# Kernel optimization log

Hardware: AMD Instinct MI355X
Metric: run time of the kernel (lower is better)

## Reference

```python
import jax, jax.numpy as jnp
import numpy as np

H, W = 64, 64
N = H * W                 # pixels
M_LOC = 2048              # unknown pixels for matting Laplacian
M_IU = 2048               # unknown pixels for intra-unknown term
NNZ_CM = 20 * N           # color-mixture nnz


def setup_inputs() -> dict:
    key = jax.random.key(0)
    k = jax.random.split(key, 15)
    inp = {}
    inp["height"] = H
    inp["width"] = W
    inp["CM_weights"] = jax.random.uniform(k[0], (N,), jnp.float32)
    inp["LOC_weights"] = jax.random.uniform(k[1], (N,), jnp.float32)
    inp["IU_weights"] = jax.random.uniform(k[2], (N,), jnp.float32)
    inp["KU_weights"] = jax.random.uniform(k[3], (N,), jnp.float32)
    inp["lmbda"] = jnp.float32(100.0)
    inp["kToUconf"] = jax.random.uniform(k[4], (N,), jnp.float32)
    inp["known"] = (jax.random.uniform(k[5], (N,)) < 0.5).astype(jnp.float32)
    inp["kToU"] = jax.random.uniform(k[6], (N,), jnp.float32)
    inp["Wcm_row"] = jax.random.randint(k[7], (NNZ_CM,), 0, N)
    inp["Wcm_col"] = jax.random.randint(k[8], (NNZ_CM,), 0, N)
    inp["Wcm_data"] = jax.random.uniform(k[9], (NNZ_CM,), jnp.float32)
    # interior pixels so all 3x3 neighbor offsets stay in [0, N)
    inp["LOC_inInd"] = jax.random.randint(k[10], (M_LOC, 1), W + 1, N - W - 1)
    inp["LOC_flows"] = jax.random.uniform(k[11], (9, 9, M_LOC), jnp.float32)
    inp["IU_inInd"] = jax.random.randint(k[12], (M_IU, 1), 0, N)
    inp["IU_flows"] = jax.random.uniform(k[13], (M_IU, 5), jnp.float32)
    inp["IU_neighInd"] = jax.random.randint(k[14], (M_IU, 5), 0, N)
    return inp


def _coo_dense(rows, cols, vals, n):
    # from_coo with duplicate (row, col) entries summed
    return jnp.zeros((n, n), vals.dtype).at[rows, cols].add(vals)


def reference(height, width, CM_weights, LOC_weights, IU_weights, KU_weights,
              lmbda, kToUconf, known, kToU, Wcm_row, Wcm_col, Wcm_data,
              LOC_inInd, LOC_flows, IU_inInd, IU_flows, IU_neighInd):
    n = height * width

    # ---- color mixture: Lcm = (diag(rowsum) - diag(cm) @ Wcm);  Lcm <- Lcm^T @ Lcm
    Wcm = _coo_dense(Wcm_row, Wcm_col, Wcm_data, n) * CM_weights[:, None]
    Lcm = jnp.diag(Wcm.sum(axis=1)) - Wcm
    Lcm = Lcm.T @ Lcm

    # ---- matting Laplacian (faithful to source: loop breaks after i == 0,
    # so only the first neighbor's rows/flows are scattered)
    w_loc = LOC_weights[LOC_inInd[:, 0]]                 # [M]
    flows = LOC_flows * w_loc[None, None, :]             # [9, 9, M]
    offs = jnp.array([-1 - width, -1, -1 + width, -width, 0, width,
                      1 - width, 1, 1 + width], dtype=LOC_inInd.dtype)
    neigh = LOC_inInd + offs[None, :]                    # [M, 9]
    m = neigh.shape[0]
    rows0 = jnp.broadcast_to(neigh[:, :1], (m, 9))       # neighInds[:, 0] tiled
    vals0 = flows[:, 0, :].T                             # [M, 9]
    Wmat = _coo_dense(rows0.reshape(-1), neigh.reshape(-1), vals0.reshape(-1), n)
    Wmat = 0.5 * (Wmat + Wmat.T)
    Lmat = jnp.diag(Wmat.sum(axis=1)) - Wmat

    # ---- intra-unknowns (5 nonlocal neighbors)
    w_iu = IU_weights[IU_inInd[:, 0]]                    # [Mi]
    f_iu = IU_flows[:, :5] * w_iu[:, None]               # [Mi, 5]
    mi = IU_inInd.shape[0]
    rows_iu = jnp.broadcast_to(IU_inInd, (mi, 5))
    Wcs = _coo_dense(rows_iu.reshape(-1), IU_neighInd[:, :5].reshape(-1),
                     f_iu.reshape(-1), n)
    Wcs = 0.5 * (Wcs + Wcs.T)
    Lcs = jnp.diag(Wcs.sum(axis=1)) - Wcs

    # ---- assemble linear system A x = b
    ku_diag = KU_weights * kToUconf
    known_diag = lmbda * known
    A = Lcs + Lmat + Lcm + jnp.diag(ku_diag + known_diag)
    b = (ku_diag + known_diag) * kToU
    return A, b
```

## Files before the change

kernel.cpp:

```cpp
#include <hip/hip_runtime.h>

#define WD 64
#define NN 4096
#define RCAP 128
#define XCAP 512

typedef float v4f __attribute__((ext_vector_type(4)));


__global__ void k_scatter(const int* __restrict__ wrow, const int* __restrict__ wcol,
                          const float* __restrict__ wdata, const float* __restrict__ cmw,
                          const int* __restrict__ locInd, const float* __restrict__ locFlows,
                          const float* __restrict__ locw,
                          const int* __restrict__ iuInd, const float* __restrict__ iuFlows,
                          const int* __restrict__ iuNeigh, const float* __restrict__ iuw,
                          int nnz, int mloc, int miu,
                          int* __restrict__ curR, int* __restrict__ curC, int* __restrict__ curX,
                          float* __restrict__ rowsum,
                          int2* __restrict__ sR, int2* __restrict__ sC, int2* __restrict__ xE) {
    int t = blockIdx.x * blockDim.x + threadIdx.x;
    if (t < nnz) {
        int r = wrow[t], c = wcol[t];
        float pos = wdata[t] * cmw[r];
        float v = -pos;
        atomicAdd(&rowsum[r], pos);
        int pR = atomicAdd(&curR[r], 1);
        if (pR < RCAP) sR[r * RCAP + pR] = make_int2(c, __float_as_int(v));
        int pC = atomicAdd(&curC[c], 1);
        if (pC < RCAP) sC[c * RCAP + pC] = make_int2(r, __float_as_int(v));
        return;
    }
    t -= nnz;
    if (t < mloc * 9) {
        int m = t / 9;
        int j = t - m * 9;
        const int offs[9] = {-1-WD, -1, -1+WD, -WD, 0, WD, 1-WD, 1, 1+WD};
        int ind = locInd[m];
        int r = ind - 1 - WD;
        int c = ind + offs[j];
        float h = 0.5f * locFlows[j * 9 * mloc + m] * locw[ind];
        int p1 = atomicAdd(&curX[r], 2);
        if (p1 + 1 < XCAP) {
            xE[r * XCAP + p1]     = make_int2(c, __float_as_int(-h));
            xE[r * XCAP + p1 + 1] = make_int2(r, __float_as_int( h));
        }
        int p2 = atomicAdd(&curX[c], 2);
        if (p2 + 1 < XCAP) {
            xE[c * XCAP + p2]     = make_int2(r, __float_as_int(-h));
            xE[c * XCAP + p2 + 1] = make_int2(c, __float_as_int( h));
        }
        return;
    }
    t -= mloc * 9;
    if (t < miu * 5) {
        int m = t / 5;
        int j = t - m * 5;
        int r = iuInd[m];
        int c = iuNeigh[m * 5 + j];
        float h = 0.5f * iuFlows[m * 5 + j] * iuw[r];
        int p1 = atomicAdd(&curX[r], 2);
        if (p1 + 1 < XCAP) {
            xE[r * XCAP + p1]     = make_int2(c, __float_as_int(-h));
            xE[r * XCAP + p1 + 1] = make_int2(r, __float_as_int( h));
        }
        int p2 = atomicAdd(&curX[c], 2);
        if (p2 + 1 < XCAP) {
            xE[c * XCAP + p2]     = make_int2(r, __float_as_int(-h));
            xE[c * XCAP + p2 + 1] = make_int2(c, __float_as_int( h));
        }
    }
}

__global__ void __launch_bounds__(256) k_rows(
    const int* __restrict__ curR, const int2* __restrict__ sR,
    const int* __restrict__ curC, const int2* __restrict__ sC,
    const int* __restrict__ curX, const int2* __restrict__ xE,
    const float* __restrict__ rowsum,
    const float* __restrict__ kuw, const float* __restrict__ conf, const float* __restrict__ known,
    const float* __restrict__ kToU, const float* __restrict__ lmbda,
    float* __restrict__ A, float* __restrict__ b) {
    __shared__ float acc[NN];
    __shared__ int   ck[RCAP + 1];
    __shared__ float cv[RCAP + 1];
    __shared__ int   crl[RCAP + 1];
    __shared__ float crs[RCAP + 1];
    int i = blockIdx.x;
    int tid = threadIdx.x;

    v4f* acc4 = (v4f*)acc;
    for (int t = tid; t < NN / 4; t += 256) acc4[t] = (v4f){0.f, 0.f, 0.f, 0.f};

    int ccnt = min(curC[i], RCAP);
    int ctot = ccnt + 1;
    for (int t = tid; t < ctot; t += 256) {
        int k; float v;
        if (t < ccnt) { int2 e = sC[i * RCAP + t]; k = e.x; v = __int_as_float(e.y); }
        else          { k = i;                     v = rowsum[i]; }
        ck[t] = k; cv[t] = v;
        crl[t] = min(curR[k], RCAP);
        crs[t] = rowsum[k];
    }
    __syncthreads();

    int wave = tid >> 6, lane = tid & 63;
    int sub = lane >> 5, hl = lane & 31;
    for (int kk = wave * 2 + sub; kk < ctot; kk += 8) {
        int k = ck[kk];
        float v = cv[kk];
        int rl = crl[kk];
        const int2* rowp = sR + k * RCAP;
        for (int t = hl; t <= rl; t += 32) {
            int j; float w;
            if (t < rl) { int2 e = rowp[t]; j = e.x; w = __int_as_float(e.y); }
            else        { j = k; w = crs[kk]; }
            atomicAdd(&acc[j], v * w);
        }
    }
    int xc = min(curX[i], XCAP);
    const int2* xp = xE + i * XCAP;
    for (int t = tid; t < xc; t += 256) {
        int2 e = xp[t];
        atomicAdd(&acc[e.x], __int_as_float(e.y));
    }
    if (tid == 0) {
        float d = kuw[i] * conf[i] + lmbda[0] * known[i];
        atomicAdd(&acc[i], d);
        b[i] = d * kToU[i];
    }
    __syncthreads();

    v4f* out4 = (v4f*)(A + (size_t)i * NN);
    for (int t = tid; t < NN / 4; t += 256)
        __builtin_nontemporal_store(acc4[t], &out4[t]);
}

extern "C" void kernel_launch(void* const* d_in, const int* in_sizes, int n_in,
                              void* d_out, int out_size, void* d_ws, size_t ws_size,
                              hipStream_t stream) {
    const float* CM_weights  = (const float*)d_in[2];
    const float* LOC_weights = (const float*)d_in[3];
    const float* IU_weights  = (const float*)d_in[4];
    const float* KU_weights  = (const float*)d_in[5];
    const float* lmbda       = (const float*)d_in[6];
    const float* kToUconf    = (const float*)d_in[7];
    const float* known       = (const float*)d_in[8];
    const float* kToU        = (const float*)d_in[9];
    const int*   Wcm_row     = (const int*)d_in[10];
    const int*   Wcm_col     = (const int*)d_in[11];
    const float* Wcm_data    = (const float*)d_in[12];
    const int*   LOC_inInd   = (const int*)d_in[13];
    const float* LOC_flows   = (const float*)d_in[14];
    const int*   IU_inInd    = (const int*)d_in[15];
    const float* IU_flows    = (const float*)d_in[16];
    const int*   IU_neighInd = (const int*)d_in[17];

    int nnz  = in_sizes[10];
    int mloc = in_sizes[13];
    int miu  = in_sizes[15];

    float* A = (float*)d_out;
    float* b = A + (size_t)NN * NN;

    int*   curR   = (int*)d_ws;
    int*   curC   = curR + NN;
    int*   curX   = curC + NN;
    float* rowsum = (float*)(curX + NN);
    int2*  sR     = (int2*)(rowsum + NN);
    int2*  sC     = sR + (size_t)NN * RCAP;
    int2*  xE     = sC + (size_t)NN * RCAP;

    (void)hipMemsetAsync(curR, 0, 4 * NN * sizeof(int), stream);

    int tt = nnz + mloc * 9 + miu * 5;
    int blks = (tt + 255) / 256;
    k_scatter<<<blks, 256, 0, stream>>>(Wcm_row, Wcm_col, Wcm_data, CM_weights,
                                        LOC_inInd, LOC_flows, LOC_weights,
                                        IU_inInd, IU_flows, IU_neighInd, IU_weights,
                                        nnz, mloc, miu, curR, curC, curX, rowsum,
                                        sR, sC, xE);
    k_rows<<<NN, 256, 0, stream>>>(curR, sR, curC, sC, curX, xE, rowsum,
                                   KU_weights, kToUconf, known, kToU, lmbda, A, b);
}
```

Baseline: 140.4 us.

## Accumulate Laplacian diagonal separately and batch scatter per source pixel

The diagonal (degree) contributions of the matting and intra-unknown terms now go into a per-pixel diagX array instead of being stored as extra edge entries. Each scatter thread handles all 9 or 5 neighbours of one source pixel and reserves its row slots with a single atomic. Row and extra-edge capacities are halved, which shrinks workspace and per-row scans. The narrower scatter work may lower parallelism, and the smaller caps could silently drop entries if a row exceeds them.

```diff
diff --git a/kernel.cpp b/kernel.cpp
--- a/kernel.cpp
+++ b/kernel.cpp
@@ -2,8 +2,8 @@
 
 #define WD 64
 #define NN 4096
-#define RCAP 128
-#define XCAP 512
+#define RCAP 64
+#define XCAP 256
 
 typedef float v4f __attribute__((ext_vector_type(4)));
 
@@ -16,7 +16,7 @@
                           const int* __restrict__ iuNeigh, const float* __restrict__ iuw,
                           int nnz, int mloc, int miu,
                           int* __restrict__ curR, int* __restrict__ curC, int* __restrict__ curX,
-                          float* __restrict__ rowsum,
+                          float* __restrict__ rowsum, float* __restrict__ diagX,
                           int2* __restrict__ sR, int2* __restrict__ sC, int2* __restrict__ xE) {
     int t = blockIdx.x * blockDim.x + threadIdx.x;
     if (t < nnz) {
@@ -31,42 +31,61 @@
         return;
     }
     t -= nnz;
-    if (t < mloc * 9) {
-        int m = t / 9;
-        int j = t - m * 9;
-        const int offs[9] = {-1-WD, -1, -1+WD, -WD, 0, WD, 1-WD, 1, 1+WD};
+    if (t < mloc) {
+        int m = t;
         int ind = locInd[m];
+        float w = locw[ind];
         int r = ind - 1 - WD;
-        int c = ind + offs[j];
-        float h = 0.5f * locFlows[j * 9 * mloc + m] * locw[ind];
-        int p1 = atomicAdd(&curX[r], 2);
-        if (p1 + 1 < XCAP) {
-            xE[r * XCAP + p1]     = make_int2(c, __float_as_int(-h));
-            xE[r * XCAP + p1 + 1] = make_int2(r, __float_as_int( h));
-        }
-        int p2 = atomicAdd(&curX[c], 2);
-        if (p2 + 1 < XCAP) {
-            xE[c * XCAP + p2]     = make_int2(r, __float_as_int(-h));
-            xE[c * XCAP + p2 + 1] = make_int2(c, __float_as_int( h));
+        int base = atomicAdd(&curX[r], 9);
+        int   cs[9];
+        float hs[9];
+        float hsum = 0.f;
+        #pragma unroll
+        for (int j = 0; j < 9; ++j) {
+            int c = ind + (j / 3 - 1) + (j % 3 - 1) * WD;
+            float h = 0.5f * locFlows[j * 9 * mloc + m] * w;
+            cs[j] = c; hs[j] = h; hsum += h;
+            if (base + j < XCAP)
+                xE[r * XCAP + base + j] = make_int2(c, __float_as_int(-h));
+        }
+        atomicAdd(&diagX[r], hsum);
+        int slots[9];
+        #pragma unroll
+        for (int j = 0; j < 9; ++j) slots[j] = atomicAdd(&curX[cs[j]], 1);
+        #pragma unroll
+        for (int j = 0; j < 9; ++j) {
+            if (slots[j] < XCAP)
+                xE[cs[j] * XCAP + slots[j]] = make_int2(r, __float_as_int(-hs[j]));
+            atomicAdd(&diagX[cs[j]], hs[j]);
         }
         return;
     }
-    t -= mloc * 9;
-    if (t < miu * 5) {
-        int m = t / 5;
-        int j = t - m * 5;
+    t -= mloc;
+    if (t < miu) {
+        int m = t;
         int r = iuInd[m];
-        int c = iuNeigh[m * 5 + j];
-        float h = 0.5f * iuFlows[m * 5 + j] * iuw[r];
-        int p1 = atomicAdd(&curX[r], 2);
-        if (p1 + 1 < XCAP) {
-            xE[r * XCAP + p1]     = make_int2(c, __float_as_int(-h));
-            xE[r * XCAP + p1 + 1] = make_int2(r, __float_as_int( h));
-        }
-        int p2 = atomicAdd(&curX[c], 2);
-        if (p2 + 1 < XCAP) {
-            xE[c * XCAP + p2]     = make_int2(r, __float_as_int(-h));
-            xE[c * XCAP + p2 + 1] = make_int2(c, __float_as_int( h));
+        float w = iuw[r];
+        int base = atomicAdd(&curX[r], 5);
+        int   cs[5];
+        float hs[5];
+        float hsum = 0.f;
+        #pragma unroll
+        for (int j = 0; j < 5; ++j) {
+            int c = iuNeigh[m * 5 + j];
+            float h = 0.5f * iuFlows[m * 5 + j] * w;
+            cs[j] = c; hs[j] = h; hsum += h;
+            if (base + j < XCAP)
+                xE[r * XCAP + base + j] = make_int2(c, __float_as_int(-h));
+        }
+        atomicAdd(&diagX[r], hsum);
+        int slots[5];
+        #pragma unroll
+        for (int j = 0; j < 5; ++j) slots[j] = atomicAdd(&curX[cs[j]], 1);
+        #pragma unroll
+        for (int j = 0; j < 5; ++j) {
+            if (slots[j] < XCAP)
+                xE[cs[j] * XCAP + slots[j]] = make_int2(r, __float_as_int(-hs[j]));
+            atomicAdd(&diagX[cs[j]], hs[j]);
         }
     }
 }
@@ -75,7 +94,7 @@
     const int* __restrict__ curR, const int2* __restrict__ sR,
     const int* __restrict__ curC, const int2* __restrict__ sC,
     const int* __restrict__ curX, const int2* __restrict__ xE,
-    const float* __restrict__ rowsum,
+    const float* __restrict__ rowsum, const float* __restrict__ diagX,
     const float* __restrict__ kuw, const float* __restrict__ conf, const float* __restrict__ known,
     const float* __restrict__ kToU, const float* __restrict__ lmbda,
     float* __restrict__ A, float* __restrict__ b) {
@@ -87,9 +106,6 @@
     int i = blockIdx.x;
     int tid = threadIdx.x;
 
-    v4f* acc4 = (v4f*)acc;
-    for (int t = tid; t < NN / 4; t += 256) acc4[t] = (v4f){0.f, 0.f, 0.f, 0.f};
-
     int ccnt = min(curC[i], RCAP);
     int ctot = ccnt + 1;
     for (int t = tid; t < ctot; t += 256) {
@@ -100,6 +116,9 @@
         crl[t] = min(curR[k], RCAP);
         crs[t] = rowsum[k];
     }
+
+    v4f* acc4 = (v4f*)acc;
+    for (int t = tid; t < NN / 4; t += 256) acc4[t] = (v4f){0.f, 0.f, 0.f, 0.f};
     __syncthreads();
 
     int wave = tid >> 6, lane = tid & 63;
@@ -124,8 +143,8 @@
     }
     if (tid == 0) {
         float d = kuw[i] * conf[i] + lmbda[0] * known[i];
-        atomicAdd(&acc[i], d);
         b[i] = d * kToU[i];
+        atomicAdd(&acc[i], d + diagX[i]);
     }
     __syncthreads();
 
@@ -165,19 +184,20 @@
     int*   curC   = curR + NN;
     int*   curX   = curC + NN;
     float* rowsum = (float*)(curX + NN);
-    int2*  sR     = (int2*)(rowsum + NN);
+    float* diagX  = rowsum + NN;
+    int2*  sR     = (int2*)(diagX + NN);
     int2*  sC     = sR + (size_t)NN * RCAP;
     int2*  xE     = sC + (size_t)NN * RCAP;
 
-    (void)hipMemsetAsync(curR, 0, 4 * NN * sizeof(int), stream);
-
-    int tt = nnz + mloc * 9 + miu * 5;
+    (void)hipMemsetAsync(curR, 0, 5 * NN * sizeof(int), stream);
+
+    int tt = nnz + mloc + miu;
     int blks = (tt + 255) / 256;
     k_scatter<<<blks, 256, 0, stream>>>(Wcm_row, Wcm_col, Wcm_data, CM_weights,
                                         LOC_inInd, LOC_flows, LOC_weights,
                                         IU_inInd, IU_flows, IU_neighInd, IU_weights,
-                                        nnz, mloc, miu, curR, curC, curX, rowsum,
+                                        nnz, mloc, miu, curR, curC, curX, rowsum, diagX,
                                         sR, sC, xE);
-    k_rows<<<NN, 256, 0, stream>>>(curR, sR, curC, sC, curX, xE, rowsum,
+    k_rows<<<NN, 256, 0, stream>>>(curR, sR, curC, sC, curX, xE, rowsum, diagX,
                                    KU_weights, kToUconf, known, kToU, lmbda, A, b);
 }
```

Measured after the change: 149.4 us. +6.5%, slower.
